# Kernel tuning notes

Hardware: AMD Instinct MI355X
Metric: run time of the kernel (lower is better)

## Reference

```python
import jax, jax.numpy as jnp
import numpy as np

NUM_EXPERTS = 16
TOP_K = 2
D_IN = 1024
D_HID = 4096
D_OUT = 1024
BATCH = 8192


def setup_inputs() -> dict:
    key = jax.random.key(0)
    ks = jax.random.split(key, 6)
    s_in = 1.0 / np.sqrt(D_IN)
    s_hid = 1.0 / np.sqrt(D_HID)
    return {
        "x": jax.random.normal(ks[0], (BATCH, D_IN), dtype=jnp.float32),
        "Wg": jax.random.normal(ks[1], (D_IN, NUM_EXPERTS), dtype=jnp.float32) * s_in,
        "W1": jax.random.normal(ks[2], (NUM_EXPERTS, D_IN, D_HID), dtype=jnp.float32) * s_in,
        "b1": jnp.zeros((NUM_EXPERTS, D_HID), dtype=jnp.float32),
        "W2": jax.random.normal(ks[3], (NUM_EXPERTS, D_HID, D_OUT), dtype=jnp.float32) * s_hid,
        "b2": jnp.zeros((NUM_EXPERTS, D_OUT), dtype=jnp.float32),
    }


def _moe_forward(x, Wg, W1, b1, W2, b2):
    # Gating: top-k routing with softmax over the selected logits.
    logits = x @ Wg                                   # [B, E]
    top_vals, top_idx = jax.lax.top_k(logits, TOP_K)  # [B, k]
    routing_weights = jax.nn.softmax(top_vals, axis=-1)  # [B, k]

    # Per-token combine weight for each expert (sum over k slots):
    # cw[b, e] = sum_k routing_weights[b, k] * (top_idx[b, k] == e)
    one_hot = jax.nn.one_hot(top_idx, NUM_EXPERTS, dtype=x.dtype)  # [B, k, E]
    combine_w = jnp.einsum("bk,bke->be", routing_weights, one_hot)  # [B, E]

    # Per-expert MLP compute + weighted scatter-add combine.
    # Fixed-size loop over experts (structurally distinct weight slices);
    # equivalent math to the original's gather/compute/scatter dispatch.
    out = jnp.zeros((x.shape[0], D_OUT), dtype=x.dtype)
    for e in range(NUM_EXPERTS):
        h = jax.nn.relu(x @ W1[e] + b1[e])            # [B, H]
        y = h @ W2[e] + b2[e]                         # [B, O]
        out = out + combine_w[:, e:e + 1] * y
    return out


def reference(x, Wg, W1, b1, W2, b2):
    return _moe_forward(x, Wg, W1, b1, W2, b2)
```

## Files before the change

### kernel.cpp

```cpp
#include <hip/hip_runtime.h>
#include <cstdio>

#define DIN   1024
#define DHID  4096
#define DOUT  1024
#define NEXP  16
#define NTOK  8192
#define NPAIR (NTOK * 2)
#define PADMAX 18432
#define MAXTILES 144

typedef _Float16 h8 __attribute__((ext_vector_type(8)));
typedef _Float16 h4 __attribute__((ext_vector_type(4)));
typedef float    f4 __attribute__((ext_vector_type(4)));

#define C_CNT  0
#define C_POFF 16
#define C_CUR  32
#define C_NT   48
#define C_TE   64
#define C_TP   256

__device__ __forceinline__ void async16(const void* g, void* l) {
  __builtin_amdgcn_global_load_lds((const __attribute__((address_space(1))) void*)g,
                                   (__attribute__((address_space(3))) void*)l, 16, 0, 0);
}

__global__ void k_init(float* __restrict__ out, const float* __restrict__ x,
                       _Float16* __restrict__ x16, int* __restrict__ ptok,
                       float* __restrict__ pw, int* __restrict__ ctrl) {
  int i = blockIdx.x * 256 + threadIdx.x;
  ((f4*)out)[i] = (f4){0.f, 0.f, 0.f, 0.f};
  float4 v = ((const float4*)x)[i];
  h4 hv = {(_Float16)v.x, (_Float16)v.y, (_Float16)v.z, (_Float16)v.w};
  ((h4*)x16)[i] = hv;
  if (i < PADMAX) { ptok[i] = 0; pw[i] = 0.f; }
  if (i < 1024) ctrl[i] = 0;
}

__global__ void k_gate(const float* __restrict__ x, const float* __restrict__ wg,
                       int* __restrict__ te, float* __restrict__ tw,
                       int* __restrict__ ctrl) {
  int t = blockIdx.x * 4 + (threadIdx.x >> 6);
  int l = threadIdx.x & 63;
  const float* xr = x + (long)t * DIN;
  float acc[NEXP];
#pragma unroll
  for (int e = 0; e < NEXP; ++e) acc[e] = 0.f;
  for (int k = l; k < DIN; k += 64) {
    float xv = xr[k];
    const float4* wr = (const float4*)(wg + (long)k * NEXP);
    float4 a = wr[0], b = wr[1], c = wr[2], d = wr[3];
    acc[0]  += xv * a.x; acc[1]  += xv * a.y; acc[2]  += xv * a.z; acc[3]  += xv * a.w;
    acc[4]  += xv * b.x; acc[5]  += xv * b.y; acc[6]  += xv * b.z; acc[7]  += xv * b.w;
    acc[8]  += xv * c.x; acc[9]  += xv * c.y; acc[10] += xv * c.z; acc[11] += xv * c.w;
    acc[12] += xv * d.x; acc[13] += xv * d.y; acc[14] += xv * d.z; acc[15] += xv * d.w;
  }
#pragma unroll
  for (int off = 32; off > 0; off >>= 1) {
#pragma unroll
    for (int e = 0; e < NEXP; ++e) acc[e] += __shfl_xor(acc[e], off, 64);
  }
  if (l == 0) {
    float v0 = -1e30f; int e0 = 0;
#pragma unroll
    for (int e = 0; e < NEXP; ++e) if (acc[e] > v0) { v0 = acc[e]; e0 = e; }
    float v1 = -1e30f; int e1 = 0;
#pragma unroll
    for (int e = 0; e < NEXP; ++e) if (e != e0 && acc[e] > v1) { v1 = acc[e]; e1 = e; }
    float d = expf(v1 - v0);
    float den = 1.f / (1.f + d);
    te[2 * t] = e0;     tw[2 * t] = den;
    te[2 * t + 1] = e1; tw[2 * t + 1] = d * den;
    atomicAdd(&ctrl[C_CNT + e0], 1);
    atomicAdd(&ctrl[C_CNT + e1], 1);
  }
}

__global__ void k_scan(int* __restrict__ ctrl) {
  if (threadIdx.x != 0) return;
  int off = 0, nt = 0;
  for (int e = 0; e < NEXP; ++e) {
    int c = ctrl[C_CNT + e];
    int tiles = (c + 127) >> 7;
    ctrl[C_POFF + e] = off;
    ctrl[C_CUR + e] = off;
    for (int i = 0; i < tiles; ++i) { ctrl[C_TE + nt] = e; ctrl[C_TP + nt] = off + i * 128; ++nt; }
    off += tiles * 128;
  }
  ctrl[C_NT] = nt;
}

__global__ void k_assign(const int* __restrict__ te, const float* __restrict__ tw,
                         int* __restrict__ ctrl, int* __restrict__ ptok,
                         float* __restrict__ pw) {
  int t = blockIdx.x * 256 + threadIdx.x;
#pragma unroll
  for (int s = 0; s < 2; ++s) {
    int e = te[2 * t + s];
    int pos = atomicAdd(&ctrl[C_CUR + e], 1);
    ptok[pos] = t;
    pw[pos] = tw[2 * t + s];
  }
}

__global__ void k_transpose(const float* __restrict__ W, _Float16* __restrict__ out,
                            int R, int C) {
  __shared__ __align__(16) _Float16 tile[64][72];
  int e = blockIdx.z;
  const float* Wb = W + ((long)e * R + blockIdx.x * 64) * C + blockIdx.y * 64;
  int tid = threadIdx.x;
  int rr = tid >> 4;
  int cc = (tid & 15) * 4;
#pragma unroll
  for (int i = 0; i < 4; ++i) {
    int r = rr + i * 16;
    float4 v = *(const float4*)(Wb + (long)r * C + cc);
    tile[cc + 0][r] = (_Float16)v.x;
    tile[cc + 1][r] = (_Float16)v.y;
    tile[cc + 2][r] = (_Float16)v.z;
    tile[cc + 3][r] = (_Float16)v.w;
  }
  __syncthreads();
  _Float16* ob = out + ((long)e * C + blockIdx.y * 64) * R + blockIdx.x * 64;
  int c2 = tid >> 3;
  int ch = tid & 7;
#pragma unroll
  for (int i = 0; i < 2; ++i) {
    int c = c2 + i * 32;
    h8 v = *(const h8*)&tile[c][ch * 8];
    *(h8*)(ob + (long)c * R + ch * 8) = v;
  }
}

template<int KD, int ND, int G1>
__global__ __launch_bounds__(256)
void k_gemm(const _Float16* __restrict__ A, const _Float16* __restrict__ Wt,
            const float* __restrict__ bias, const int* __restrict__ ctrl,
            const int* __restrict__ ptok, const float* __restrict__ pw,
            _Float16* __restrict__ Hout, float* __restrict__ out) {
  __shared__ __align__(16) _Float16 As[128 * 64];
  __shared__ __align__(16) _Float16 Bs[128 * 64];
  int mt = blockIdx.y;
  if (mt >= ctrl[C_NT]) return;
  int e  = ctrl[C_TE + mt];
  int p0 = ctrl[C_TP + mt];
  int n0 = blockIdx.x * 128;
  int tid = threadIdx.x;
  int w = tid >> 6, l = tid & 63;
  int wm = w & 1, wn = w >> 1;
  int ln15 = l & 15, lq = l >> 4;

  const _Float16* ag[4];
  const _Float16* bg[4];
#pragma unroll
  for (int j = 0; j < 4; ++j) {
    int r = (w * 4 + j) * 8 + (l >> 3);
    int c = (l & 7) ^ (r & 7);
    long arow = G1 ? (long)ptok[p0 + r] : (long)(p0 + r);
    ag[j] = A + arow * KD + c * 8;
    bg[j] = Wt + ((long)e * ND + n0 + r) * KD + c * 8;
  }

  f4 acc[4][4];
#pragma unroll
  for (int i = 0; i < 4; ++i)
#pragma unroll
    for (int j = 0; j < 4; ++j) acc[i][j] = (f4){0.f, 0.f, 0.f, 0.f};

  for (int k0 = 0; k0 < KD; k0 += 64) {
#pragma unroll
    for (int j = 0; j < 4; ++j) {
      async16(ag[j] + k0, &As[(w * 4 + j) * 512]);
      async16(bg[j] + k0, &Bs[(w * 4 + j) * 512]);
    }
    __syncthreads();
#pragma unroll
    for (int ks = 0; ks < 2; ++ks) {
      h8 af[4], bf[4];
      int kq = ks * 4 + lq;
#pragma unroll
      for (int i = 0; i < 4; ++i) {
        int m = wm * 64 + i * 16 + ln15;
        af[i] = *(const h8*)&As[m * 64 + (kq ^ (m & 7)) * 8];
      }
#pragma unroll
      for (int j = 0; j < 4; ++j) {
        int n = wn * 64 + j * 16 + ln15;
        bf[j] = *(const h8*)&Bs[n * 64 + (kq ^ (n & 7)) * 8];
      }
#pragma unroll
      for (int i = 0; i < 4; ++i)
#pragma unroll
        for (int j = 0; j < 4; ++j)
          acc[i][j] = __builtin_amdgcn_mfma_f32_16x16x32_f16(af[i], bf[j], acc[i][j], 0, 0, 0);
    }
    __syncthreads();
  }

  float bj[4];
#pragma unroll
  for (int j = 0; j < 4; ++j) bj[j] = bias[e * ND + n0 + wn * 64 + j * 16 + ln15];

  if (G1) {
#pragma unroll
    for (int i = 0; i < 4; ++i)
#pragma unroll
      for (int reg = 0; reg < 4; ++reg) {
        int p = p0 + wm * 64 + i * 16 + lq * 4 + reg;
        _Float16* hr = Hout + (long)p * DHID + n0 + wn * 64 + ln15;
#pragma unroll
        for (int j = 0; j < 4; ++j)
          hr[j * 16] = (_Float16)fmaxf(acc[i][j][reg] + bj[j], 0.f);
      }
  } else {
#pragma unroll
    for (int i = 0; i < 4; ++i)
#pragma unroll
      for (int reg = 0; reg < 4; ++reg) {
        int p = p0 + wm * 64 + i * 16 + lq * 4 + reg;
        float wgt = pw[p];
        if (wgt != 0.f) {
          int t = ptok[p];
          float* orow = out + (long)t * DOUT + n0 + wn * 64 + ln15;
#pragma unroll
          for (int j = 0; j < 4; ++j)
            atomicAdd(&orow[j * 16], wgt * (acc[i][j][reg] + bj[j]));
        }
      }
  }
}

extern "C" void kernel_launch(void* const* d_in, const int* in_sizes, int n_in,
                              void* d_out, int out_size, void* d_ws, size_t ws_size,
                              hipStream_t stream) {
  const float* x  = (const float*)d_in[0];
  const float* Wg = (const float*)d_in[1];
  const float* W1 = (const float*)d_in[2];
  const float* b1 = (const float*)d_in[3];
  const float* W2 = (const float*)d_in[4];
  const float* b2 = (const float*)d_in[5];
  float* out = (float*)d_out;
  char* ws = (char*)d_ws;

  size_t WT_OFF = 0;
  size_t H_OFF  = WT_OFF + (size_t)NEXP * DHID * DIN * 2;
  size_t X_OFF  = H_OFF  + (size_t)PADMAX * DHID * 2;
  size_t TE_OFF = X_OFF  + (size_t)NTOK * DIN * 2;
  size_t TW_OFF = TE_OFF + (size_t)NPAIR * 4;
  size_t PT_OFF = TW_OFF + (size_t)NPAIR * 4;
  size_t PW_OFF = PT_OFF + (size_t)PADMAX * 4;
  size_t CT_OFF = PW_OFF + (size_t)PADMAX * 4;
  size_t END    = CT_OFF + 4096;
  if (ws_size < END) {
    fprintf(stderr, "kernel_launch: ws too small (%zu < %zu)\n", ws_size, END);
    return;
  }
  _Float16* Wt  = (_Float16*)(ws + WT_OFF);
  _Float16* H   = (_Float16*)(ws + H_OFF);
  _Float16* x16 = (_Float16*)(ws + X_OFF);
  int*   te   = (int*)(ws + TE_OFF);
  float* tw   = (float*)(ws + TW_OFF);
  int*   pt   = (int*)(ws + PT_OFF);
  float* pw   = (float*)(ws + PW_OFF);
  int*   ctrl = (int*)(ws + CT_OFF);

  k_init<<<NTOK * DIN / (256 * 4), 256, 0, stream>>>(out, x, x16, pt, pw, ctrl);
  k_gate<<<NTOK / 4, 256, 0, stream>>>(x, Wg, te, tw, ctrl);
  k_scan<<<1, 64, 0, stream>>>(ctrl);
  k_assign<<<NTOK / 256, 256, 0, stream>>>(te, tw, ctrl, pt, pw);

  k_transpose<<<dim3(DIN / 64, DHID / 64, NEXP), 256, 0, stream>>>(W1, Wt, DIN, DHID);
  k_gemm<DIN, DHID, 1><<<dim3(DHID / 128, MAXTILES), 256, 0, stream>>>(
      x16, Wt, b1, ctrl, pt, pw, H, nullptr);

  k_transpose<<<dim3(DHID / 64, DOUT / 64, NEXP), 256, 0, stream>>>(W2, Wt, DHID, DOUT);
  k_gemm<DHID, DOUT, 0><<<dim3(DOUT / 128, MAXTILES), 256, 0, stream>>>(
      H, Wt, b2, ctrl, pt, pw, nullptr, out);
}
```

Baseline: 1.365 ms.

## Double-buffer GEMM LDS, stage H stores, widen transpose tiles, parallelize scan

The expert GEMM kernel now keeps two LDS buffers, issuing async global-to-LDS loads for the next K step while MFMAs run on the current one. The first GEMM's output goes through LDS so H is written as coalesced 16-byte rows instead of scattered half stores. The weight transpose handles 128-row tiles per block, and the tile-table fill in the scan kernel is spread across 256 threads. The costs are doubled LDS use per block (64KB), which may reduce occupancy, and more code complexity.

After: 1.307 ms. 4.2% less time.

```diff
diff --git a/kernel.cpp b/kernel.cpp
--- a/kernel.cpp
+++ b/kernel.cpp
@@ -78,17 +78,30 @@
 }
 
 __global__ void k_scan(int* __restrict__ ctrl) {
-  if (threadIdx.x != 0) return;
-  int off = 0, nt = 0;
-  for (int e = 0; e < NEXP; ++e) {
-    int c = ctrl[C_CNT + e];
-    int tiles = (c + 127) >> 7;
-    ctrl[C_POFF + e] = off;
-    ctrl[C_CUR + e] = off;
-    for (int i = 0; i < tiles; ++i) { ctrl[C_TE + nt] = e; ctrl[C_TP + nt] = off + i * 128; ++nt; }
-    off += tiles * 128;
-  }
-  ctrl[C_NT] = nt;
+  __shared__ int sOff[NEXP], sT0[NEXP], sTiles[NEXP];
+  int tid = threadIdx.x;
+  if (tid == 0) {
+    int off = 0, nt = 0;
+    for (int e = 0; e < NEXP; ++e) {
+      int c = ctrl[C_CNT + e];
+      int tiles = (c + 127) >> 7;
+      ctrl[C_POFF + e] = off;
+      ctrl[C_CUR + e] = off;
+      sOff[e] = off; sT0[e] = nt; sTiles[e] = tiles;
+      nt += tiles;
+      off += tiles * 128;
+    }
+    ctrl[C_NT] = nt;
+  }
+  __syncthreads();
+  int nt = sT0[NEXP - 1] + sTiles[NEXP - 1];
+  for (int j = tid; j < nt; j += blockDim.x) {
+    int e = 0;
+#pragma unroll
+    for (int k = 1; k < NEXP; ++k) if (j >= sT0[k]) e = k;
+    ctrl[C_TE + j] = e;
+    ctrl[C_TP + j] = sOff[e] + (j - sT0[e]) * 128;
+  }
 }
 
 __global__ void k_assign(const int* __restrict__ te, const float* __restrict__ tw,
@@ -106,14 +119,14 @@
 
 __global__ void k_transpose(const float* __restrict__ W, _Float16* __restrict__ out,
                             int R, int C) {
-  __shared__ __align__(16) _Float16 tile[64][72];
+  __shared__ __align__(16) _Float16 tile[64][136];
   int e = blockIdx.z;
-  const float* Wb = W + ((long)e * R + blockIdx.x * 64) * C + blockIdx.y * 64;
+  const float* Wb = W + ((long)e * R + blockIdx.x * 128) * C + blockIdx.y * 64;
   int tid = threadIdx.x;
   int rr = tid >> 4;
   int cc = (tid & 15) * 4;
 #pragma unroll
-  for (int i = 0; i < 4; ++i) {
+  for (int i = 0; i < 8; ++i) {
     int r = rr + i * 16;
     float4 v = *(const float4*)(Wb + (long)r * C + cc);
     tile[cc + 0][r] = (_Float16)v.x;
@@ -122,14 +135,13 @@
     tile[cc + 3][r] = (_Float16)v.w;
   }
   __syncthreads();
-  _Float16* ob = out + ((long)e * C + blockIdx.y * 64) * R + blockIdx.x * 64;
-  int c2 = tid >> 3;
-  int ch = tid & 7;
-#pragma unroll
-  for (int i = 0; i < 2; ++i) {
-    int c = c2 + i * 32;
-    h8 v = *(const h8*)&tile[c][ch * 8];
-    *(h8*)(ob + (long)c * R + ch * 8) = v;
+  _Float16* ob = out + ((long)e * C + blockIdx.y * 64) * R + blockIdx.x * 128;
+  int c2 = tid >> 4;
+  int ch = tid & 15;
+#pragma unroll
+  for (int i = 0; i < 4; ++i) {
+    int c = c2 + i * 16;
+    *(h8*)(ob + (long)c * R + ch * 8) = *(const h8*)&tile[c][ch * 8];
   }
 }
 
@@ -139,8 +151,12 @@
             const float* __restrict__ bias, const int* __restrict__ ctrl,
             const int* __restrict__ ptok, const float* __restrict__ pw,
             _Float16* __restrict__ Hout, float* __restrict__ out) {
-  __shared__ __align__(16) _Float16 As[128 * 64];
-  __shared__ __align__(16) _Float16 Bs[128 * 64];
+  __shared__ __align__(16) _Float16 sm[32768];
+  _Float16* As0 = sm;
+  _Float16* Bs0 = sm + 8192;
+  _Float16* As1 = sm + 16384;
+  _Float16* Bs1 = sm + 24576;
+
   int mt = blockIdx.y;
   if (mt >= ctrl[C_NT]) return;
   int e  = ctrl[C_TE + mt];
@@ -168,13 +184,14 @@
 #pragma unroll
     for (int j = 0; j < 4; ++j) acc[i][j] = (f4){0.f, 0.f, 0.f, 0.f};
 
-  for (int k0 = 0; k0 < KD; k0 += 64) {
+  auto stage = [&](int k0, _Float16* A_, _Float16* B_) {
 #pragma unroll
     for (int j = 0; j < 4; ++j) {
-      async16(ag[j] + k0, &As[(w * 4 + j) * 512]);
-      async16(bg[j] + k0, &Bs[(w * 4 + j) * 512]);
+      async16(ag[j] + k0, A_ + (w * 4 + j) * 512);
+      async16(bg[j] + k0, B_ + (w * 4 + j) * 512);
     }
-    __syncthreads();
+  };
+  auto compute = [&](const _Float16* A_, const _Float16* B_) {
 #pragma unroll
     for (int ks = 0; ks < 2; ++ks) {
       h8 af[4], bf[4];
@@ -182,12 +199,12 @@
 #pragma unroll
       for (int i = 0; i < 4; ++i) {
         int m = wm * 64 + i * 16 + ln15;
-        af[i] = *(const h8*)&As[m * 64 + (kq ^ (m & 7)) * 8];
+        af[i] = *(const h8*)&A_[m * 64 + (kq ^ (m & 7)) * 8];
       }
 #pragma unroll
       for (int j = 0; j < 4; ++j) {
         int n = wn * 64 + j * 16 + ln15;
-        bf[j] = *(const h8*)&Bs[n * 64 + (kq ^ (n & 7)) * 8];
+        bf[j] = *(const h8*)&B_[n * 64 + (kq ^ (n & 7)) * 8];
       }
 #pragma unroll
       for (int i = 0; i < 4; ++i)
@@ -195,7 +212,19 @@
         for (int j = 0; j < 4; ++j)
           acc[i][j] = __builtin_amdgcn_mfma_f32_16x16x32_f16(af[i], bf[j], acc[i][j], 0, 0, 0);
     }
+  };
+
+  constexpr int KSTEPS = KD / 64;
+  stage(0, As0, Bs0);
+  __syncthreads();
+#pragma unroll 1
+  for (int t = 0; t < KSTEPS; t += 2) {
+    stage((t + 1) * 64, As1, Bs1);
+    compute(As0, Bs0);
     __syncthreads();
+    if (t + 2 < KSTEPS) stage((t + 2) * 64, As0, Bs0);
+    compute(As1, Bs1);
+    __syncthreads();
   }
 
   float bj[4];
@@ -207,12 +236,20 @@
     for (int i = 0; i < 4; ++i)
 #pragma unroll
       for (int reg = 0; reg < 4; ++reg) {
-        int p = p0 + wm * 64 + i * 16 + lq * 4 + reg;
-        _Float16* hr = Hout + (long)p * DHID + n0 + wn * 64 + ln15;
+        int row = wm * 64 + i * 16 + lq * 4 + reg;
 #pragma unroll
         for (int j = 0; j < 4; ++j)
-          hr[j * 16] = (_Float16)fmaxf(acc[i][j][reg] + bj[j], 0.f);
+          sm[row * 136 + wn * 64 + j * 16 + ln15] =
+              (_Float16)fmaxf(acc[i][j][reg] + bj[j], 0.f);
       }
+    __syncthreads();
+#pragma unroll
+    for (int p = 0; p < 8; ++p) {
+      int idx = p * 256 + tid;
+      int row = idx >> 4, ch = idx & 15;
+      *(h8*)(Hout + (long)(p0 + row) * DHID + n0 + ch * 8) =
+          *(const h8*)&sm[row * 136 + ch * 8];
+    }
   } else {
 #pragma unroll
     for (int i = 0; i < 4; ++i)
@@ -267,14 +304,14 @@
 
   k_init<<<NTOK * DIN / (256 * 4), 256, 0, stream>>>(out, x, x16, pt, pw, ctrl);
   k_gate<<<NTOK / 4, 256, 0, stream>>>(x, Wg, te, tw, ctrl);
-  k_scan<<<1, 64, 0, stream>>>(ctrl);
+  k_scan<<<1, 256, 0, stream>>>(ctrl);
   k_assign<<<NTOK / 256, 256, 0, stream>>>(te, tw, ctrl, pt, pw);
 
-  k_transpose<<<dim3(DIN / 64, DHID / 64, NEXP), 256, 0, stream>>>(W1, Wt, DIN, DHID);
+  k_transpose<<<dim3(DIN / 128, DHID / 64, NEXP), 256, 0, stream>>>(W1, Wt, DIN, DHID);
   k_gemm<DIN, DHID, 1><<<dim3(DHID / 128, MAXTILES), 256, 0, stream>>>(
       x16, Wt, b1, ctrl, pt, pw, H, nullptr);
 
-  k_transpose<<<dim3(DHID / 64, DOUT / 64, NEXP), 256, 0, stream>>>(W2, Wt, DHID, DOUT);
+  k_transpose<<<dim3(DHID / 128, DOUT / 64, NEXP), 256, 0, stream>>>(W2, Wt, DHID, DOUT);
   k_gemm<DHID, DOUT, 0><<<dim3(DOUT / 128, MAXTILES), 256, 0, stream>>>(
       H, Wt, b2, ctrl, pt, pw, nullptr, out);
 }
```
